# Performance work log

Measured on AMD Instinct MI355X. Metric: run time of the kernel, lower is better.

The kernel has to match this reference:

```python
import jax, jax.numpy as jnp
import numpy as np

N = 500_000          # num nodes
K = 3                # neighbors per star subgraph = graphlet_size - 1
E = N * K            # one subgraph per node -> directed (center, nbr) edges
L = 2                # hop_neighbor
FD = 2               # final_dim = 2**pqc_dim
H = 64               # hidden_dim
NC = 8               # num_classes
NIN = 16             # node_input_dim
EIN = 8              # edge_input_dim


def _lin(k, i, o):
    # torch.nn.Linear-style init scale
    return jax.random.normal(k, (i, o), jnp.float32) * (1.0 / np.sqrt(i))


def setup_inputs() -> dict:
    key = jax.random.key(0)
    ks = jax.random.split(key, 32)
    node_feat = jax.random.normal(ks[0], (N, NIN), jnp.float32)
    edge_attr = jax.random.normal(ks[1], (E, EIN), jnp.float32)
    # edge e = (center, neighbor); centers grouped: edges 3i..3i+2 belong to node i
    centers = jnp.repeat(jnp.arange(N, dtype=jnp.int32), K)
    neighbors = jax.random.randint(ks[2], (E,), 0, N, dtype=jnp.int32)
    edge_index = jnp.stack([centers, neighbors])  # [2, E]
    batch = jnp.zeros((N,), jnp.int32)
    msg_W1 = jnp.stack([_lin(ks[6 + i], 2 * FD, H) for i in range(L)])
    msg_W2 = jnp.stack([_lin(ks[8 + i], H, FD) for i in range(L)])
    upd_W1 = jnp.stack([_lin(ks[10 + i], 2 * FD, H) for i in range(L)])
    upd_W2 = jnp.stack([_lin(ks[12 + i], H, FD) for i in range(L)])
    return dict(
        node_feat=node_feat, edge_attr=edge_attr, edge_index=edge_index, batch=batch,
        Wn=_lin(ks[3], NIN, FD), bn=jnp.zeros((FD,), jnp.float32),
        We=_lin(ks[4], EIN, FD), be=jnp.zeros((FD,), jnp.float32),
        msg_W1=msg_W1, msg_b1=jnp.zeros((L, H), jnp.float32),
        msg_W2=msg_W2, msg_b2=jnp.zeros((L, FD), jnp.float32),
        upd_W1=upd_W1, upd_b1=jnp.zeros((L, H), jnp.float32),
        upd_W2=upd_W2, upd_b2=jnp.zeros((L, FD), jnp.float32),
        fin_W1=_lin(ks[14], FD, H), fin_b1=jnp.zeros((H,), jnp.float32),
        fin_W2=_lin(ks[15], H, NC), fin_b2=jnp.zeros((NC,), jnp.float32),
    )


def _leaky(x):
    return jnp.where(x >= 0, x, 0.1 * x)


def _mlp(x, W1, b1, W2, b2):
    # MLP([din, 64, dout], act=LeakyReLU(0.1)); dropout inactive at eval
    return _leaky(x @ W1 + b1) @ W2 + b2


def reference(node_feat, edge_attr, edge_index, batch, Wn, bn, We, be,
              msg_W1, msg_b1, msg_W2, msg_b2, upd_W1, upd_b1, upd_W2, upd_b2,
              fin_W1, fin_b1, fin_W2, fin_b2):
    ctr = edge_index[0]  # [E] center of each star edge
    nbr = edge_index[1]  # [E] neighbor
    h = node_feat @ Wn + bn      # [N, FD] input_node projection
    e = edge_attr @ We + be      # [E, FD] input_edge projection (fixed across layers)
    for l in range(L):
        # message over each (center, neighbor) edge: concat(edge_feat, nbr_feat)
        msg = _mlp(jnp.concatenate([e, h[nbr]], axis=1),
                   msg_W1[l], msg_b1[l], msg_W2[l], msg_b2[l])  # [E, FD]
        aggr = jax.ops.segment_sum(msg, ctr, num_segments=N)    # [N, FD]
        new = _mlp(jnp.concatenate([h, aggr], axis=1),
                   upd_W1[l], upd_b1[l], upd_W2[l], upd_b2[l])  # [N, FD]
        h = jax.nn.relu(h + new)  # updates_node[center] += new_center; then ReLU
    return _mlp(h, fin_W1, fin_b1, fin_W2, fin_b2)  # [N, NC]
```

## Files before the change

### kernel.cpp

```cpp
#include <hip/hip_runtime.h>

#define NN 500000
#define KK 3
#define EE (NN * KK)
#define HH 64
#define NC 8
#define NIN 16
#define EIN 8

typedef __attribute__((ext_vector_type(2))) _Float16 h2;
typedef __attribute__((ext_vector_type(2)))  float sf2;
typedef __attribute__((ext_vector_type(8)))  float sf8;
typedef __attribute__((ext_vector_type(16))) float sf16;

using pk_t = decltype(__builtin_amdgcn_cvt_pkrtz(0.f, 0.f));

#if __has_builtin(__builtin_elementwise_fma)
#define PKFMA(a,b,c) __builtin_elementwise_fma((a),(b),(c))
#else
#define PKFMA(a,b,c) ((a)*(b)+(c))
#endif

__device__ __forceinline__ h2 bch2(float f)        { return __builtin_bit_cast(h2, f); }
__device__ __forceinline__ h2 bch2u(unsigned int u){ return __builtin_bit_cast(h2, u); }
__device__ __forceinline__ h2 dup16(float f) {
    return __builtin_bit_cast(h2, __builtin_amdgcn_cvt_pkrtz(f, f));
}
__device__ __forceinline__ unsigned int pkrtz_u(float a, float b) {
    return __builtin_bit_cast(unsigned int, __builtin_amdgcn_cvt_pkrtz(a, b));
}
__device__ __forceinline__ h2 splat_lo(unsigned int u) {
    h2 p = bch2u(u); h2 r; r.x = p.x; r.y = p.x; return r;
}
__device__ __forceinline__ h2 splat_hi(unsigned int u) {
    h2 p = bch2u(u); h2 r; r.x = p.y; r.y = p.y; return r;
}
__device__ __forceinline__ float lo_f32(unsigned int u) { return (float)bch2u(u).x; }
__device__ __forceinline__ float hi_f32(unsigned int u) { return (float)bch2u(u).y; }

__device__ __forceinline__ float fdot2(h2 a, h2 b, float c) {
#if __has_builtin(__builtin_amdgcn_fdot2)
    return __builtin_amdgcn_fdot2(__builtin_bit_cast(pk_t, a),
                                  __builtin_bit_cast(pk_t, b), c, false);
#else
    return c + (float)a.x * (float)b.x + (float)a.y * (float)b.y;
#endif
}
__device__ __forceinline__ h2 lk2(h2 x) {
    h2 c = {(_Float16)0.1f, (_Float16)0.1f};
    return __builtin_elementwise_max(x, x * c);
}
__device__ __forceinline__ float pack2(float a, float b) {
    h2 v; v.x = (_Float16)a; v.y = (_Float16)b;
    return __builtin_bit_cast(float, v);
}

__global__ __launch_bounds__(256) void prep_kernel(
    const float* __restrict__ node_feat,
    const float* __restrict__ Wn, const float* __restrict__ bn,
    unsigned int* __restrict__ hp,
    const float* __restrict__ msgW1, const float* __restrict__ msgb1, const float* __restrict__ msgW2,
    const float* __restrict__ updW1, const float* __restrict__ updb1, const float* __restrict__ updW2,
    const float* __restrict__ finW1, const float* __restrict__ finb1, const float* __restrict__ finW2,
    float* __restrict__ wpack)
{
    const sf16* Wn16 = (const sf16*)Wn;
    sf16 wn0 = Wn16[0];
    sf16 wn1 = Wn16[1];
    sf2  bnv = ((const sf2*)bn)[0];

    int idx = blockIdx.x * 256 + threadIdx.x;
    if (idx < NN) {
        const float4* x4 = (const float4*)(node_feat + (size_t)idx * NIN);
        float4 v0 = x4[0], v1 = x4[1], v2 = x4[2], v3 = x4[3];
        float xs[16] = {v0.x, v0.y, v0.z, v0.w, v1.x, v1.y, v1.z, v1.w,
                        v2.x, v2.y, v2.z, v2.w, v3.x, v3.y, v3.z, v3.w};
        float a0 = bnv.x, a1 = bnv.y;
#pragma unroll
        for (int i = 0; i < 8; i++) {
            a0 = fmaf(xs[i], wn0[2 * i], a0);
            a1 = fmaf(xs[i], wn0[2 * i + 1], a1);
        }
#pragma unroll
        for (int i = 0; i < 8; i++) {
            a0 = fmaf(xs[8 + i], wn1[2 * i], a0);
            a1 = fmaf(xs[8 + i], wn1[2 * i + 1], a1);
        }
        hp[idx] = pkrtz_u(a0, a1);
    }

    if (blockIdx.x == 0) {
        int t = threadIdx.x;
        if (t < 32) {
            int l = t >> 4, which = (t >> 3) & 1, c = t & 7;
            const float* W1 = (which ? updW1 : msgW1) + l * 4 * HH;
            const float* b1 = (which ? updb1 : msgb1) + l * HH;
            const float* W2 = (which ? updW2 : msgW2) + l * 2 * HH;
            float* dst = wpack + (l * 2 + which) * 256 + c * 32;
            int j0 = c * 8;
            for (int r = 0; r < 4; r++)
                for (int p = 0; p < 4; p++)
                    dst[r * 4 + p] = pack2(W1[r * HH + j0 + 2 * p], W1[r * HH + j0 + 2 * p + 1]);
            for (int p = 0; p < 4; p++) {
                dst[16 + p] = pack2(b1[j0 + 2 * p], b1[j0 + 2 * p + 1]);
                dst[20 + p] = pack2(W2[(j0 + 2 * p) * 2 + 0], W2[(j0 + 2 * p + 1) * 2 + 0]);
                dst[24 + p] = pack2(W2[(j0 + 2 * p) * 2 + 1], W2[(j0 + 2 * p + 1) * 2 + 1]);
                dst[28 + p] = 0.0f;
            }
        } else if (t < 40) {
            int c = t - 32, j0 = c * 8;
            float* dst = wpack + 1024 + c * 48;
            for (int p = 0; p < 4; p++) {
                dst[p]      = pack2(finW1[j0 + 2 * p],      finW1[j0 + 2 * p + 1]);
                dst[4 + p]  = pack2(finW1[HH + j0 + 2 * p], finW1[HH + j0 + 2 * p + 1]);
                dst[8 + p]  = pack2(finb1[j0 + 2 * p],      finb1[j0 + 2 * p + 1]);
                dst[12 + p] = 0.0f;
            }
            for (int jp = 0; jp < 4; jp++)
                for (int cc = 0; cc < NC; cc++)
                    dst[16 + jp * 8 + cc] = pack2(finW2[(j0 + 2 * jp) * NC + cc],
                                                  finW2[(j0 + 2 * jp + 1) * NC + cc]);
        }
    }
}

__global__ __launch_bounds__(256) void layer0_kernel(
    const unsigned int* __restrict__ hp_in,
    const float* __restrict__ edge_attr,
    const float* __restrict__ We, const float* __restrict__ be,
    const int* __restrict__ nbr,
    const float* __restrict__ mblk, const float* __restrict__ mb2,
    const float* __restrict__ ublk, const float* __restrict__ ub2,
    unsigned int* __restrict__ hp_out, unsigned int* __restrict__ ep_out)
{
    int i = blockIdx.x * 256 + threadIdx.x;
    if (i >= NN) return;

    sf16 wev = ((const sf16*)We)[0];
    sf2  bev = ((const sf2*)be)[0];
    sf2  mb2v = ((const sf2*)mb2)[0];
    sf2  ub2v = ((const sf2*)ub2)[0];

    int base = i * KK;

    h2 ex[3], ey[3];
#pragma unroll
    for (int k = 0; k < 3; k++) {
        const float4* x4 = (const float4*)(edge_attr + (size_t)(base + k) * EIN);
        float4 v0 = x4[0], v1 = x4[1];
        float xs[8] = {v0.x, v0.y, v0.z, v0.w, v1.x, v1.y, v1.z, v1.w};
        float a0 = bev.x, a1 = bev.y;
#pragma unroll
        for (int q = 0; q < 8; q++) {
            a0 = fmaf(xs[q], wev[2 * q], a0);
            a1 = fmaf(xs[q], wev[2 * q + 1], a1);
        }
        ep_out[base + k] = pkrtz_u(a0, a1);
        ex[k] = dup16(a0); ey[k] = dup16(a1);
    }

    unsigned int hO = hp_in[i];
    int n0 = nbr[base + 0], n1 = nbr[base + 1], n2 = nbr[base + 2];
    unsigned int g0 = hp_in[n0], g1 = hp_in[n1], g2 = hp_in[n2];

    h2 n0x = splat_lo(g0), n0y = splat_hi(g0);
    h2 n1x = splat_lo(g1), n1y = splat_hi(g1);
    h2 n2x = splat_lo(g2), n2y = splat_hi(g2);

    const sf16* M = (const sf16*)mblk;
    const sf16* U = (const sf16*)ublk;

    float a0 = 3.0f * mb2v.x, a1 = 3.0f * mb2v.y;
#pragma unroll 2
    for (int c = 0; c < 8; c++) {
        sf16 A = M[2 * c];
        sf16 B = M[2 * c + 1];
#pragma unroll
        for (int jp = 0; jp < 4; jp++) {
            h2 w0 = bch2(A[jp]), w1 = bch2(A[4 + jp]);
            h2 w2 = bch2(A[8 + jp]), w3 = bch2(A[12 + jp]);
            h2 bb = bch2(B[jp]);
            h2 t0 = PKFMA(ex[0], w0, PKFMA(ey[0], w1, PKFMA(n0x, w2, PKFMA(n0y, w3, bb))));
            h2 t1 = PKFMA(ex[1], w0, PKFMA(ey[1], w1, PKFMA(n1x, w2, PKFMA(n1y, w3, bb))));
            h2 t2 = PKFMA(ex[2], w0, PKFMA(ey[2], w1, PKFMA(n2x, w2, PKFMA(n2y, w3, bb))));
            h2 ts = lk2(t0) + lk2(t1) + lk2(t2);
            a0 = fdot2(ts, bch2(B[4 + jp]), a0);
            a1 = fdot2(ts, bch2(B[8 + jp]), a1);
        }
    }

    h2 hx = splat_lo(hO), hy = splat_hi(hO);
    h2 ax = dup16(a0), ay = dup16(a1);
    float u0 = ub2v.x, u1 = ub2v.y;
#pragma unroll 2
    for (int c = 0; c < 8; c++) {
        sf16 A = U[2 * c];
        sf16 B = U[2 * c + 1];
#pragma unroll
        for (int jp = 0; jp < 4; jp++) {
            h2 tt = PKFMA(hx, bch2(A[jp]),
                    PKFMA(hy, bch2(A[4 + jp]),
                    PKFMA(ax, bch2(A[8 + jp]),
                    PKFMA(ay, bch2(A[12 + jp]), bch2(B[jp])))));
            tt = lk2(tt);
            u0 = fdot2(tt, bch2(B[4 + jp]), u0);
            u1 = fdot2(tt, bch2(B[8 + jp]), u1);
        }
    }
    float nh0 = fmaxf(lo_f32(hO) + u0, 0.0f);
    float nh1 = fmaxf(hi_f32(hO) + u1, 0.0f);
    hp_out[i] = pkrtz_u(nh0, nh1);
}

__global__ __launch_bounds__(256) void layer1_kernel(
    const unsigned int* __restrict__ hp_in, const unsigned int* __restrict__ eP,
    const int* __restrict__ nbr,
    const float* __restrict__ mblk, const float* __restrict__ mb2,
    const float* __restrict__ ublk, const float* __restrict__ ub2,
    const float* __restrict__ fblk, const float* __restrict__ fb2,
    float* __restrict__ out)
{
    int i = blockIdx.x * 256 + threadIdx.x;
    if (i >= NN) return;

    sf2 mb2v = ((const sf2*)mb2)[0];
    sf2 ub2v = ((const sf2*)ub2)[0];

    unsigned int hO = hp_in[i];
    int base = i * KK;
    int n0 = nbr[base + 0], n1 = nbr[base + 1], n2 = nbr[base + 2];
    unsigned int g0 = hp_in[n0], g1 = hp_in[n1], g2 = hp_in[n2];
    unsigned int e0 = eP[base + 0], e1 = eP[base + 1], e2 = eP[base + 2];

    h2 e0x = splat_lo(e0), e0y = splat_hi(e0);
    h2 e1x = splat_lo(e1), e1y = splat_hi(e1);
    h2 e2x = splat_lo(e2), e2y = splat_hi(e2);
    h2 n0x = splat_lo(g0), n0y = splat_hi(g0);
    h2 n1x = splat_lo(g1), n1y = splat_hi(g1);
    h2 n2x = splat_lo(g2), n2y = splat_hi(g2);

    const sf16* M = (const sf16*)mblk;
    const sf16* U = (const sf16*)ublk;

    float a0 = 3.0f * mb2v.x, a1 = 3.0f * mb2v.y;
#pragma unroll 2
    for (int c = 0; c < 8; c++) {
        sf16 A = M[2 * c];
        sf16 B = M[2 * c + 1];
#pragma unroll
        for (int jp = 0; jp < 4; jp++) {
            h2 w0 = bch2(A[jp]), w1 = bch2(A[4 + jp]);
            h2 w2 = bch2(A[8 + jp]), w3 = bch2(A[12 + jp]);
            h2 bb = bch2(B[jp]);
            h2 t0 = PKFMA(e0x, w0, PKFMA(e0y, w1, PKFMA(n0x, w2, PKFMA(n0y, w3, bb))));
            h2 t1 = PKFMA(e1x, w0, PKFMA(e1y, w1, PKFMA(n1x, w2, PKFMA(n1y, w3, bb))));
            h2 t2 = PKFMA(e2x, w0, PKFMA(e2y, w1, PKFMA(n2x, w2, PKFMA(n2y, w3, bb))));
            h2 ts = lk2(t0) + lk2(t1) + lk2(t2);
            a0 = fdot2(ts, bch2(B[4 + jp]), a0);
            a1 = fdot2(ts, bch2(B[8 + jp]), a1);
        }
    }

    h2 hx = splat_lo(hO), hy = splat_hi(hO);
    h2 ax = dup16(a0), ay = dup16(a1);
    float u0 = ub2v.x, u1 = ub2v.y;
#pragma unroll 2
    for (int c = 0; c < 8; c++) {
        sf16 A = U[2 * c];
        sf16 B = U[2 * c + 1];
#pragma unroll
        for (int jp = 0; jp < 4; jp++) {
            h2 tt = PKFMA(hx, bch2(A[jp]),
                    PKFMA(hy, bch2(A[4 + jp]),
                    PKFMA(ax, bch2(A[8 + jp]),
                    PKFMA(ay, bch2(A[12 + jp]), bch2(B[jp])))));
            tt = lk2(tt);
            u0 = fdot2(tt, bch2(B[4 + jp]), u0);
            u1 = fdot2(tt, bch2(B[8 + jp]), u1);
        }
    }
    float nh0 = fmaxf(lo_f32(hO) + u0, 0.0f);
    float nh1 = fmaxf(hi_f32(hO) + u1, 0.0f);

    sf8 fb2v = ((const sf8*)fb2)[0];
    float o[NC];
#pragma unroll
    for (int cc = 0; cc < NC; cc++) o[cc] = fb2v[cc];
    h2 nx = dup16(nh0), ny = dup16(nh1);
#pragma unroll 2
    for (int c = 0; c < 8; c++) {
        const float* F = fblk + c * 48;
        sf16 A = ((const sf16*)F)[0];
        sf16 B = ((const sf16*)F)[1];
        sf16 C = ((const sf16*)F)[2];
#pragma unroll
        for (int jp = 0; jp < 4; jp++) {
            h2 w1a = bch2(A[jp]), w1b = bch2(A[4 + jp]), bb = bch2(A[8 + jp]);
            h2 tt = lk2(PKFMA(nx, w1a, PKFMA(ny, w1b, bb)));
#pragma unroll
            for (int cc = 0; cc < NC; cc++) {
                float w = (jp < 2) ? B[(jp & 1) * 8 + cc] : C[(jp & 1) * 8 + cc];
                o[cc] = fdot2(tt, bch2(w), o[cc]);
            }
        }
    }
    float4* op = (float4*)(out + (size_t)i * NC);
    op[0] = make_float4(o[0], o[1], o[2], o[3]);
    op[1] = make_float4(o[4], o[5], o[6], o[7]);
}

extern "C" void kernel_launch(void* const* d_in, const int* in_sizes, int n_in,
                              void* d_out, int out_size, void* d_ws, size_t ws_size,
                              hipStream_t stream) {
    const float* node_feat = (const float*)d_in[0];
    const float* edge_attr = (const float*)d_in[1];
    const int* edge_index = (const int*)d_in[2];
    const float* Wn = (const float*)d_in[4];
    const float* bn = (const float*)d_in[5];
    const float* We = (const float*)d_in[6];
    const float* be = (const float*)d_in[7];
    const float* msgW1 = (const float*)d_in[8];
    const float* msgb1 = (const float*)d_in[9];
    const float* msgW2 = (const float*)d_in[10];
    const float* msgb2 = (const float*)d_in[11];
    const float* updW1 = (const float*)d_in[12];
    const float* updb1 = (const float*)d_in[13];
    const float* updW2 = (const float*)d_in[14];
    const float* updb2 = (const float*)d_in[15];
    const float* finW1 = (const float*)d_in[16];
    const float* finb1 = (const float*)d_in[17];
    const float* finW2 = (const float*)d_in[18];
    const float* finb2 = (const float*)d_in[19];
    float* out = (float*)d_out;

    const int* nbr = edge_index + EE;

    char* ws = (char*)d_ws;
    unsigned int* hA = (unsigned int*)ws;
    unsigned int* hB = (unsigned int*)(ws + (size_t)NN * 4);
    unsigned int* eP = (unsigned int*)(ws + (size_t)NN * 8);
    float* wpack = (float*)(ws + (size_t)NN * 8 + (size_t)EE * 4);

    const int threads = 256;
    int grid = (NN + threads - 1) / threads;

    prep_kernel<<<grid, threads, 0, stream>>>(
        node_feat, Wn, bn, hA,
        msgW1, msgb1, msgW2, updW1, updb1, updW2,
        finW1, finb1, finW2, wpack);

    layer0_kernel<<<grid, threads, 0, stream>>>(
        hA, edge_attr, We, be, nbr,
        wpack + 0 * 256, msgb2,
        wpack + 1 * 256, updb2,
        hB, eP);

    layer1_kernel<<<grid, threads, 0, stream>>>(
        hB, eP, nbr,
        wpack + 2 * 256, msgb2 + 2,
        wpack + 3 * 256, updb2 + 2,
        wpack + 1024, finb2, out);
}
```

Before: 193.1 us.

## Fuse prep and both layers into one cooperative persistent kernel with grid syncs

Replaces the three launches (prep, layer0, layer1) with a single cooperative kernel of 1024 blocks that processes two nodes per thread, separated by grid-wide syncs. Per-node state (own h, edge projections, neighbor indices) stays in registers across layers, so the edge-projection buffer is no longer written and re-read, and launch gaps disappear. The cost is grid.sync overhead and lower occupancy from the persistent grid and extra live registers. If cooperative launch is unavailable or fails, it falls back to the old three-kernel path.

```diff
diff --git a/kernel.cpp b/kernel.cpp
--- a/kernel.cpp
+++ b/kernel.cpp
@@ -1,4 +1,7 @@
 #include <hip/hip_runtime.h>
+#include <hip/hip_cooperative_groups.h>
+
+namespace cg = cooperative_groups;
 
 #define NN 500000
 #define KK 3
@@ -8,6 +11,10 @@
 #define NIN 16
 #define EIN 8
 
+#define NBLK 1024
+#define NTHR 256
+#define STRIDE (NBLK * NTHR)
+
 typedef __attribute__((ext_vector_type(2))) _Float16 h2;
 typedef __attribute__((ext_vector_type(2)))  float sf2;
 typedef __attribute__((ext_vector_type(8)))  float sf8;
@@ -55,182 +62,16 @@
     return __builtin_bit_cast(float, v);
 }
 
-__global__ __launch_bounds__(256) void prep_kernel(
-    const float* __restrict__ node_feat,
-    const float* __restrict__ Wn, const float* __restrict__ bn,
-    unsigned int* __restrict__ hp,
-    const float* __restrict__ msgW1, const float* __restrict__ msgb1, const float* __restrict__ msgW2,
-    const float* __restrict__ updW1, const float* __restrict__ updb1, const float* __restrict__ updW2,
-    const float* __restrict__ finW1, const float* __restrict__ finb1, const float* __restrict__ finW2,
-    float* __restrict__ wpack)
-{
-    const sf16* Wn16 = (const sf16*)Wn;
-    sf16 wn0 = Wn16[0];
-    sf16 wn1 = Wn16[1];
-    sf2  bnv = ((const sf2*)bn)[0];
-
-    int idx = blockIdx.x * 256 + threadIdx.x;
-    if (idx < NN) {
-        const float4* x4 = (const float4*)(node_feat + (size_t)idx * NIN);
-        float4 v0 = x4[0], v1 = x4[1], v2 = x4[2], v3 = x4[3];
-        float xs[16] = {v0.x, v0.y, v0.z, v0.w, v1.x, v1.y, v1.z, v1.w,
-                        v2.x, v2.y, v2.z, v2.w, v3.x, v3.y, v3.z, v3.w};
-        float a0 = bnv.x, a1 = bnv.y;
-#pragma unroll
-        for (int i = 0; i < 8; i++) {
-            a0 = fmaf(xs[i], wn0[2 * i], a0);
-            a1 = fmaf(xs[i], wn0[2 * i + 1], a1);
-        }
-#pragma unroll
-        for (int i = 0; i < 8; i++) {
-            a0 = fmaf(xs[8 + i], wn1[2 * i], a0);
-            a1 = fmaf(xs[8 + i], wn1[2 * i + 1], a1);
-        }
-        hp[idx] = pkrtz_u(a0, a1);
-    }
-
-    if (blockIdx.x == 0) {
-        int t = threadIdx.x;
-        if (t < 32) {
-            int l = t >> 4, which = (t >> 3) & 1, c = t & 7;
-            const float* W1 = (which ? updW1 : msgW1) + l * 4 * HH;
-            const float* b1 = (which ? updb1 : msgb1) + l * HH;
-            const float* W2 = (which ? updW2 : msgW2) + l * 2 * HH;
-            float* dst = wpack + (l * 2 + which) * 256 + c * 32;
-            int j0 = c * 8;
-            for (int r = 0; r < 4; r++)
-                for (int p = 0; p < 4; p++)
-                    dst[r * 4 + p] = pack2(W1[r * HH + j0 + 2 * p], W1[r * HH + j0 + 2 * p + 1]);
-            for (int p = 0; p < 4; p++) {
-                dst[16 + p] = pack2(b1[j0 + 2 * p], b1[j0 + 2 * p + 1]);
-                dst[20 + p] = pack2(W2[(j0 + 2 * p) * 2 + 0], W2[(j0 + 2 * p + 1) * 2 + 0]);
-                dst[24 + p] = pack2(W2[(j0 + 2 * p) * 2 + 1], W2[(j0 + 2 * p + 1) * 2 + 1]);
-                dst[28 + p] = 0.0f;
-            }
-        } else if (t < 40) {
-            int c = t - 32, j0 = c * 8;
-            float* dst = wpack + 1024 + c * 48;
-            for (int p = 0; p < 4; p++) {
-                dst[p]      = pack2(finW1[j0 + 2 * p],      finW1[j0 + 2 * p + 1]);
-                dst[4 + p]  = pack2(finW1[HH + j0 + 2 * p], finW1[HH + j0 + 2 * p + 1]);
-                dst[8 + p]  = pack2(finb1[j0 + 2 * p],      finb1[j0 + 2 * p + 1]);
-                dst[12 + p] = 0.0f;
-            }
-            for (int jp = 0; jp < 4; jp++)
-                for (int cc = 0; cc < NC; cc++)
-                    dst[16 + jp * 8 + cc] = pack2(finW2[(j0 + 2 * jp) * NC + cc],
-                                                  finW2[(j0 + 2 * jp + 1) * NC + cc]);
-        }
-    }
-}
-
-__global__ __launch_bounds__(256) void layer0_kernel(
-    const unsigned int* __restrict__ hp_in,
-    const float* __restrict__ edge_attr,
-    const float* __restrict__ We, const float* __restrict__ be,
-    const int* __restrict__ nbr,
+
+__device__ __forceinline__ unsigned int layer_math(
+    unsigned int hO,
+    unsigned int e0, unsigned int e1, unsigned int e2,
+    unsigned int g0, unsigned int g1, unsigned int g2,
     const float* __restrict__ mblk, const float* __restrict__ mb2,
-    const float* __restrict__ ublk, const float* __restrict__ ub2,
-    unsigned int* __restrict__ hp_out, unsigned int* __restrict__ ep_out)
-{
-    int i = blockIdx.x * 256 + threadIdx.x;
-    if (i >= NN) return;
-
-    sf16 wev = ((const sf16*)We)[0];
-    sf2  bev = ((const sf2*)be)[0];
-    sf2  mb2v = ((const sf2*)mb2)[0];
-    sf2  ub2v = ((const sf2*)ub2)[0];
-
-    int base = i * KK;
-
-    h2 ex[3], ey[3];
-#pragma unroll
-    for (int k = 0; k < 3; k++) {
-        const float4* x4 = (const float4*)(edge_attr + (size_t)(base + k) * EIN);
-        float4 v0 = x4[0], v1 = x4[1];
-        float xs[8] = {v0.x, v0.y, v0.z, v0.w, v1.x, v1.y, v1.z, v1.w};
-        float a0 = bev.x, a1 = bev.y;
-#pragma unroll
-        for (int q = 0; q < 8; q++) {
-            a0 = fmaf(xs[q], wev[2 * q], a0);
-            a1 = fmaf(xs[q], wev[2 * q + 1], a1);
-        }
-        ep_out[base + k] = pkrtz_u(a0, a1);
-        ex[k] = dup16(a0); ey[k] = dup16(a1);
-    }
-
-    unsigned int hO = hp_in[i];
-    int n0 = nbr[base + 0], n1 = nbr[base + 1], n2 = nbr[base + 2];
-    unsigned int g0 = hp_in[n0], g1 = hp_in[n1], g2 = hp_in[n2];
-
-    h2 n0x = splat_lo(g0), n0y = splat_hi(g0);
-    h2 n1x = splat_lo(g1), n1y = splat_hi(g1);
-    h2 n2x = splat_lo(g2), n2y = splat_hi(g2);
-
-    const sf16* M = (const sf16*)mblk;
-    const sf16* U = (const sf16*)ublk;
-
-    float a0 = 3.0f * mb2v.x, a1 = 3.0f * mb2v.y;
-#pragma unroll 2
-    for (int c = 0; c < 8; c++) {
-        sf16 A = M[2 * c];
-        sf16 B = M[2 * c + 1];
-#pragma unroll
-        for (int jp = 0; jp < 4; jp++) {
-            h2 w0 = bch2(A[jp]), w1 = bch2(A[4 + jp]);
-            h2 w2 = bch2(A[8 + jp]), w3 = bch2(A[12 + jp]);
-            h2 bb = bch2(B[jp]);
-            h2 t0 = PKFMA(ex[0], w0, PKFMA(ey[0], w1, PKFMA(n0x, w2, PKFMA(n0y, w3, bb))));
-            h2 t1 = PKFMA(ex[1], w0, PKFMA(ey[1], w1, PKFMA(n1x, w2, PKFMA(n1y, w3, bb))));
-            h2 t2 = PKFMA(ex[2], w0, PKFMA(ey[2], w1, PKFMA(n2x, w2, PKFMA(n2y, w3, bb))));
-            h2 ts = lk2(t0) + lk2(t1) + lk2(t2);
-            a0 = fdot2(ts, bch2(B[4 + jp]), a0);
-            a1 = fdot2(ts, bch2(B[8 + jp]), a1);
-        }
-    }
-
-    h2 hx = splat_lo(hO), hy = splat_hi(hO);
-    h2 ax = dup16(a0), ay = dup16(a1);
-    float u0 = ub2v.x, u1 = ub2v.y;
-#pragma unroll 2
-    for (int c = 0; c < 8; c++) {
-        sf16 A = U[2 * c];
-        sf16 B = U[2 * c + 1];
-#pragma unroll
-        for (int jp = 0; jp < 4; jp++) {
-            h2 tt = PKFMA(hx, bch2(A[jp]),
-                    PKFMA(hy, bch2(A[4 + jp]),
-                    PKFMA(ax, bch2(A[8 + jp]),
-                    PKFMA(ay, bch2(A[12 + jp]), bch2(B[jp])))));
-            tt = lk2(tt);
-            u0 = fdot2(tt, bch2(B[4 + jp]), u0);
-            u1 = fdot2(tt, bch2(B[8 + jp]), u1);
-        }
-    }
-    float nh0 = fmaxf(lo_f32(hO) + u0, 0.0f);
-    float nh1 = fmaxf(hi_f32(hO) + u1, 0.0f);
-    hp_out[i] = pkrtz_u(nh0, nh1);
-}
-
-__global__ __launch_bounds__(256) void layer1_kernel(
-    const unsigned int* __restrict__ hp_in, const unsigned int* __restrict__ eP,
-    const int* __restrict__ nbr,
-    const float* __restrict__ mblk, const float* __restrict__ mb2,
-    const float* __restrict__ ublk, const float* __restrict__ ub2,
-    const float* __restrict__ fblk, const float* __restrict__ fb2,
-    float* __restrict__ out)
-{
-    int i = blockIdx.x * 256 + threadIdx.x;
-    if (i >= NN) return;
-
+    const float* __restrict__ ublk, const float* __restrict__ ub2)
+{
     sf2 mb2v = ((const sf2*)mb2)[0];
     sf2 ub2v = ((const sf2*)ub2)[0];
-
-    unsigned int hO = hp_in[i];
-    int base = i * KK;
-    int n0 = nbr[base + 0], n1 = nbr[base + 1], n2 = nbr[base + 2];
-    unsigned int g0 = hp_in[n0], g1 = hp_in[n1], g2 = hp_in[n2];
-    unsigned int e0 = eP[base + 0], e1 = eP[base + 1], e2 = eP[base + 2];
 
     h2 e0x = splat_lo(e0), e0y = splat_hi(e0);
     h2 e1x = splat_lo(e1), e1y = splat_hi(e1);
@@ -281,12 +122,19 @@
     }
     float nh0 = fmaxf(lo_f32(hO) + u0, 0.0f);
     float nh1 = fmaxf(hi_f32(hO) + u1, 0.0f);
-
+    return pkrtz_u(nh0, nh1);
+}
+
+__device__ __forceinline__ void final_math(
+    unsigned int hU,
+    const float* __restrict__ fblk, const float* __restrict__ fb2,
+    float* __restrict__ outp)
+{
     sf8 fb2v = ((const sf8*)fb2)[0];
     float o[NC];
 #pragma unroll
     for (int cc = 0; cc < NC; cc++) o[cc] = fb2v[cc];
-    h2 nx = dup16(nh0), ny = dup16(nh1);
+    h2 nx = splat_lo(hU), ny = splat_hi(hU);
 #pragma unroll 2
     for (int c = 0; c < 8; c++) {
         const float* F = fblk + c * 48;
@@ -304,9 +152,259 @@
             }
         }
     }
-    float4* op = (float4*)(out + (size_t)i * NC);
+    float4* op = (float4*)outp;
     op[0] = make_float4(o[0], o[1], o[2], o[3]);
     op[1] = make_float4(o[4], o[5], o[6], o[7]);
+}
+
+__device__ __forceinline__ void p1_node(
+    int i,
+    const float* __restrict__ node_feat, const float* __restrict__ edge_attr,
+    const int* __restrict__ nbr,
+    sf16 wn0, sf16 wn1, sf2 bnv, sf16 wev, sf2 bev,
+    unsigned int* __restrict__ hA,
+    unsigned int& hs, unsigned int* ep, int* nb)
+{
+    const float4* x4 = (const float4*)(node_feat + (size_t)i * NIN);
+    float4 v0 = x4[0], v1 = x4[1], v2 = x4[2], v3 = x4[3];
+    float xs[16] = {v0.x, v0.y, v0.z, v0.w, v1.x, v1.y, v1.z, v1.w,
+                    v2.x, v2.y, v2.z, v2.w, v3.x, v3.y, v3.z, v3.w};
+    float a0 = bnv.x, a1 = bnv.y;
+#pragma unroll
+    for (int q = 0; q < 8; q++) {
+        a0 = fmaf(xs[q], wn0[2 * q], a0);
+        a1 = fmaf(xs[q], wn0[2 * q + 1], a1);
+    }
+#pragma unroll
+    for (int q = 0; q < 8; q++) {
+        a0 = fmaf(xs[8 + q], wn1[2 * q], a0);
+        a1 = fmaf(xs[8 + q], wn1[2 * q + 1], a1);
+    }
+    hs = pkrtz_u(a0, a1);
+    hA[i] = hs;
+
+    int base = i * KK;
+    nb[0] = nbr[base + 0];
+    nb[1] = nbr[base + 1];
+    nb[2] = nbr[base + 2];
+
+#pragma unroll
+    for (int k = 0; k < 3; k++) {
+        const float4* e4 = (const float4*)(edge_attr + (size_t)(base + k) * EIN);
+        float4 w0 = e4[0], w1 = e4[1];
+        float es[8] = {w0.x, w0.y, w0.z, w0.w, w1.x, w1.y, w1.z, w1.w};
+        float b0 = bev.x, b1 = bev.y;
+#pragma unroll
+        for (int q = 0; q < 8; q++) {
+            b0 = fmaf(es[q], wev[2 * q], b0);
+            b1 = fmaf(es[q], wev[2 * q + 1], b1);
+        }
+        ep[k] = pkrtz_u(b0, b1);
+    }
+}
+
+__device__ __forceinline__ void pack_weights(
+    int t,
+    const float* __restrict__ msgW1, const float* __restrict__ msgb1, const float* __restrict__ msgW2,
+    const float* __restrict__ updW1, const float* __restrict__ updb1, const float* __restrict__ updW2,
+    const float* __restrict__ finW1, const float* __restrict__ finb1, const float* __restrict__ finW2,
+    float* __restrict__ wpack)
+{
+    if (t < 32) {
+        int l = t >> 4, which = (t >> 3) & 1, c = t & 7;
+        const float* W1 = (which ? updW1 : msgW1) + l * 4 * HH;
+        const float* b1 = (which ? updb1 : msgb1) + l * HH;
+        const float* W2 = (which ? updW2 : msgW2) + l * 2 * HH;
+        float* dst = wpack + (l * 2 + which) * 256 + c * 32;
+        int j0 = c * 8;
+        for (int r = 0; r < 4; r++)
+            for (int p = 0; p < 4; p++)
+                dst[r * 4 + p] = pack2(W1[r * HH + j0 + 2 * p], W1[r * HH + j0 + 2 * p + 1]);
+        for (int p = 0; p < 4; p++) {
+            dst[16 + p] = pack2(b1[j0 + 2 * p], b1[j0 + 2 * p + 1]);
+            dst[20 + p] = pack2(W2[(j0 + 2 * p) * 2 + 0], W2[(j0 + 2 * p + 1) * 2 + 0]);
+            dst[24 + p] = pack2(W2[(j0 + 2 * p) * 2 + 1], W2[(j0 + 2 * p + 1) * 2 + 1]);
+            dst[28 + p] = 0.0f;
+        }
+    } else if (t < 40) {
+        int c = t - 32, j0 = c * 8;
+        float* dst = wpack + 1024 + c * 48;
+        for (int p = 0; p < 4; p++) {
+            dst[p]      = pack2(finW1[j0 + 2 * p],      finW1[j0 + 2 * p + 1]);
+            dst[4 + p]  = pack2(finW1[HH + j0 + 2 * p], finW1[HH + j0 + 2 * p + 1]);
+            dst[8 + p]  = pack2(finb1[j0 + 2 * p],      finb1[j0 + 2 * p + 1]);
+            dst[12 + p] = 0.0f;
+        }
+        for (int jp = 0; jp < 4; jp++)
+            for (int cc = 0; cc < NC; cc++)
+                dst[16 + jp * 8 + cc] = pack2(finW2[(j0 + 2 * jp) * NC + cc],
+                                              finW2[(j0 + 2 * jp + 1) * NC + cc]);
+    }
+}
+
+__global__ __launch_bounds__(NTHR, 4) void fused_kernel(
+    const float* __restrict__ node_feat, const float* __restrict__ edge_attr,
+    const int* __restrict__ nbr,
+    const float* __restrict__ Wn, const float* __restrict__ bn,
+    const float* __restrict__ We, const float* __restrict__ be,
+    const float* __restrict__ msgW1, const float* __restrict__ msgb1,
+    const float* __restrict__ msgW2, const float* __restrict__ msgb2,
+    const float* __restrict__ updW1, const float* __restrict__ updb1,
+    const float* __restrict__ updW2, const float* __restrict__ updb2,
+    const float* __restrict__ finW1, const float* __restrict__ finb1,
+    const float* __restrict__ finW2, const float* __restrict__ finb2,
+    unsigned int* __restrict__ hA, unsigned int* __restrict__ hB,
+    float* __restrict__ wpack, float* __restrict__ out)
+{
+    cg::grid_group grid = cg::this_grid();
+    int tid = blockIdx.x * NTHR + threadIdx.x;
+
+    unsigned int hs[2] = {0u, 0u};
+    unsigned int ep[2][3] = {{0u,0u,0u},{0u,0u,0u}};
+    int nb[2][3] = {{0,0,0},{0,0,0}};
+
+    {
+        const sf16* Wn16 = (const sf16*)Wn;
+        sf16 wn0 = Wn16[0], wn1 = Wn16[1];
+        sf2  bnv = ((const sf2*)bn)[0];
+        sf16 wev = ((const sf16*)We)[0];
+        sf2  bev = ((const sf2*)be)[0];
+#pragma unroll
+        for (int n = 0; n < 2; n++) {
+            int i = tid + n * STRIDE;
+            if (i < NN)
+                p1_node(i, node_feat, edge_attr, nbr, wn0, wn1, bnv, wev, bev,
+                        hA, hs[n], ep[n], nb[n]);
+        }
+        if (blockIdx.x == 0)
+            pack_weights(threadIdx.x, msgW1, msgb1, msgW2,
+                         updW1, updb1, updW2, finW1, finb1, finW2, wpack);
+    }
+
+    grid.sync();
+
+#pragma unroll
+    for (int n = 0; n < 2; n++) {
+        int i = tid + n * STRIDE;
+        if (i < NN) {
+            unsigned int g0 = hA[nb[n][0]], g1 = hA[nb[n][1]], g2 = hA[nb[n][2]];
+            hs[n] = layer_math(hs[n], ep[n][0], ep[n][1], ep[n][2], g0, g1, g2,
+                               wpack + 0 * 256, msgb2, wpack + 1 * 256, updb2);
+            hB[i] = hs[n];
+        }
+    }
+
+    grid.sync();
+
+#pragma unroll
+    for (int n = 0; n < 2; n++) {
+        int i = tid + n * STRIDE;
+        if (i < NN) {
+            unsigned int g0 = hB[nb[n][0]], g1 = hB[nb[n][1]], g2 = hB[nb[n][2]];
+            unsigned int hU = layer_math(hs[n], ep[n][0], ep[n][1], ep[n][2], g0, g1, g2,
+                                         wpack + 2 * 256, msgb2 + 2, wpack + 3 * 256, updb2 + 2);
+            final_math(hU, wpack + 1024, finb2, out + (size_t)i * NC);
+        }
+    }
+}
+
+__global__ __launch_bounds__(256) void prep_kernel(
+    const float* __restrict__ node_feat,
+    const float* __restrict__ Wn, const float* __restrict__ bn,
+    unsigned int* __restrict__ hp,
+    const float* __restrict__ msgW1, const float* __restrict__ msgb1, const float* __restrict__ msgW2,
+    const float* __restrict__ updW1, const float* __restrict__ updb1, const float* __restrict__ updW2,
+    const float* __restrict__ finW1, const float* __restrict__ finb1, const float* __restrict__ finW2,
+    float* __restrict__ wpack)
+{
+    const sf16* Wn16 = (const sf16*)Wn;
+    sf16 wn0 = Wn16[0];
+    sf16 wn1 = Wn16[1];
+    sf2  bnv = ((const sf2*)bn)[0];
+
+    int idx = blockIdx.x * 256 + threadIdx.x;
+    if (idx < NN) {
+        const float4* x4 = (const float4*)(node_feat + (size_t)idx * NIN);
+        float4 v0 = x4[0], v1 = x4[1], v2 = x4[2], v3 = x4[3];
+        float xs[16] = {v0.x, v0.y, v0.z, v0.w, v1.x, v1.y, v1.z, v1.w,
+                        v2.x, v2.y, v2.z, v2.w, v3.x, v3.y, v3.z, v3.w};
+        float a0 = bnv.x, a1 = bnv.y;
+#pragma unroll
+        for (int i = 0; i < 8; i++) {
+            a0 = fmaf(xs[i], wn0[2 * i], a0);
+            a1 = fmaf(xs[i], wn0[2 * i + 1], a1);
+        }
+#pragma unroll
+        for (int i = 0; i < 8; i++) {
+            a0 = fmaf(xs[8 + i], wn1[2 * i], a0);
+            a1 = fmaf(xs[8 + i], wn1[2 * i + 1], a1);
+        }
+        hp[idx] = pkrtz_u(a0, a1);
+    }
+
+    if (blockIdx.x == 0)
+        pack_weights(threadIdx.x, msgW1, msgb1, msgW2,
+                     updW1, updb1, updW2, finW1, finb1, finW2, wpack);
+}
+
+__global__ __launch_bounds__(256) void layer0_kernel(
+    const unsigned int* __restrict__ hp_in,
+    const float* __restrict__ edge_attr,
+    const float* __restrict__ We, const float* __restrict__ be,
+    const int* __restrict__ nbr,
+    const float* __restrict__ mblk, const float* __restrict__ mb2,
+    const float* __restrict__ ublk, const float* __restrict__ ub2,
+    unsigned int* __restrict__ hp_out, unsigned int* __restrict__ ep_out)
+{
+    int i = blockIdx.x * 256 + threadIdx.x;
+    if (i >= NN) return;
+
+    sf16 wev = ((const sf16*)We)[0];
+    sf2  bev = ((const sf2*)be)[0];
+
+    int base = i * KK;
+    unsigned int epk[3];
+#pragma unroll
+    for (int k = 0; k < 3; k++) {
+        const float4* x4 = (const float4*)(edge_attr + (size_t)(base + k) * EIN);
+        float4 v0 = x4[0], v1 = x4[1];
+        float xs[8] = {v0.x, v0.y, v0.z, v0.w, v1.x, v1.y, v1.z, v1.w};
+        float a0 = bev.x, a1 = bev.y;
+#pragma unroll
+        for (int q = 0; q < 8; q++) {
+            a0 = fmaf(xs[q], wev[2 * q], a0);
+            a1 = fmaf(xs[q], wev[2 * q + 1], a1);
+        }
+        epk[k] = pkrtz_u(a0, a1);
+        ep_out[base + k] = epk[k];
+    }
+
+    unsigned int hO = hp_in[i];
+    int n0 = nbr[base + 0], n1 = nbr[base + 1], n2 = nbr[base + 2];
+    unsigned int g0 = hp_in[n0], g1 = hp_in[n1], g2 = hp_in[n2];
+
+    hp_out[i] = layer_math(hO, epk[0], epk[1], epk[2], g0, g1, g2, mblk, mb2, ublk, ub2);
+}
+
+__global__ __launch_bounds__(256) void layer1_kernel(
+    const unsigned int* __restrict__ hp_in, const unsigned int* __restrict__ eP,
+    const int* __restrict__ nbr,
+    const float* __restrict__ mblk, const float* __restrict__ mb2,
+    const float* __restrict__ ublk, const float* __restrict__ ub2,
+    const float* __restrict__ fblk, const float* __restrict__ fb2,
+    float* __restrict__ out)
+{
+    int i = blockIdx.x * 256 + threadIdx.x;
+    if (i >= NN) return;
+
+    unsigned int hO = hp_in[i];
+    int base = i * KK;
+    int n0 = nbr[base + 0], n1 = nbr[base + 1], n2 = nbr[base + 2];
+    unsigned int g0 = hp_in[n0], g1 = hp_in[n1], g2 = hp_in[n2];
+    unsigned int e0 = eP[base + 0], e1 = eP[base + 1], e2 = eP[base + 2];
+
+    unsigned int hU = layer_math(hO, e0, e1, e2, g0, g1, g2, mblk, mb2, ublk, ub2);
+    final_math(hU, fblk, fb2, out + (size_t)i * NC);
 }
 
 extern "C" void kernel_launch(void* const* d_in, const int* in_sizes, int n_in,
@@ -341,6 +439,30 @@
     unsigned int* eP = (unsigned int*)(ws + (size_t)NN * 8);
     float* wpack = (float*)(ws + (size_t)NN * 8 + (size_t)EE * 4);
 
+    static int coop_ok = -1;
+    if (coop_ok < 0) {
+        int v = 0;
+        if (hipDeviceGetAttribute(&v, hipDeviceAttributeCooperativeLaunch, 0) != hipSuccess)
+            v = 0;
+        coop_ok = v;
+    }
+
+    if (coop_ok) {
+        void* args[] = {
+            (void*)&node_feat, (void*)&edge_attr, (void*)&nbr,
+            (void*)&Wn, (void*)&bn, (void*)&We, (void*)&be,
+            (void*)&msgW1, (void*)&msgb1, (void*)&msgW2, (void*)&msgb2,
+            (void*)&updW1, (void*)&updb1, (void*)&updW2, (void*)&updb2,
+            (void*)&finW1, (void*)&finb1, (void*)&finW2, (void*)&finb2,
+            (void*)&hA, (void*)&hB, (void*)&wpack, (void*)&out
+        };
+        hipError_t err = hipLaunchCooperativeKernel((const void*)fused_kernel,
+                                                    dim3(NBLK), dim3(NTHR),
+                                                    args, 0, stream);
+        if (err == hipSuccess) return;
+        coop_ok = 0;
+    }
+
     const int threads = 256;
     int grid = (NN + threads - 1) / threads;
 
```

Result: no change. 190.9 us (-1.2%).
